# Kernel tuning notes

Hardware: AMD Instinct MI355X
Metric: run time of the kernel (lower is better)

Reference implementation:

```python
import jax, jax.numpy as jnp
import numpy as np

B, S, C = 16, 1024, 1024
E, H = 1024, 16
DH = E // H

def setup_inputs() -> dict:
    key = jax.random.key(0)
    k1, k2, k3, k4, k5 = jax.random.split(key, 5)
    x = jax.random.normal(k1, (B, S, C), dtype=jnp.float32)
    # learned params, sized per init_kwargs (torch Linear default init scale ~ 1/sqrt(fan_in))
    w_qkv = jax.random.normal(k2, (C, 3 * E), dtype=jnp.float32) / np.sqrt(C)
    b_qkv = jax.random.normal(k3, (3 * E,), dtype=jnp.float32) * 0.01
    w_o = jax.random.normal(k4, (E, E), dtype=jnp.float32) / np.sqrt(E)
    b_o = jax.random.normal(k5, (E,), dtype=jnp.float32) * 0.01
    return {"x": x, "w_qkv": w_qkv, "b_qkv": b_qkv, "w_o": w_o, "b_o": b_o}

def reference(x, w_qkv, b_qkv, w_o, b_o):
    b, s, _ = x.shape
    # fused QKV projection: [B,S,3E] -> [B,S,H,3*Dh]
    qkv = (jnp.einsum('bsc,ce->bse', x, w_qkv) + b_qkv).reshape(b, s, H, 3 * DH)
    q, k, v = jnp.split(qkv, 3, axis=-1)  # each [B,S,H,Dh]
    # NOTE: faithful to source — attention over the HEADS axis at each position,
    # scaled by embed_size**-0.5 (not head_dim).
    attn = jnp.einsum('bshd,bstd->bsht', q, k) * (E ** -0.5)  # [B,S,H,H]
    attn = jax.nn.softmax(attn, axis=-1)
    out = jnp.einsum('bsht,bstd->bshd', attn, v).reshape(b, s, E)
    return jnp.einsum('bse,ef->bsf', out, w_o) + b_o
```

## Files before the change

### kernel.cpp

```cpp
#include <hip/hip_runtime.h>
#include <hip/hip_bf16.h>
#include <stdint.h>

#define DEVINLINE __device__ __forceinline__

typedef __attribute__((ext_vector_type(4))) float f32x4;
typedef __attribute__((ext_vector_type(8))) short bf16x8;

DEVINLINE unsigned short f2bf(float f) {
    union { float f; uint32_t u; } v; v.f = f;
    uint32_t u = v.u;
    uint32_t rounding = 0x7FFFu + ((u >> 16) & 1u);
    u += rounding;
    return (unsigned short)(u >> 16);
}

DEVINLINE float bf2f(unsigned short h) {
    union { uint32_t u; float f; } v; v.u = ((uint32_t)h) << 16;
    return v.f;
}

__global__ void cvt_f32_bf16(const float* __restrict__ in,
                             unsigned short* __restrict__ out, int n) {
    int i = (blockIdx.x * blockDim.x + threadIdx.x) * 4;
    int stride = gridDim.x * blockDim.x * 4;
    for (; i < n; i += stride) {
        float4 v = *reinterpret_cast<const float4*>(in + i);
        ushort4 o;
        o.x = f2bf(v.x); o.y = f2bf(v.y); o.z = f2bf(v.z); o.w = f2bf(v.w);
        *reinterpret_cast<ushort4*>(out + i) = o;
    }
}

__global__ void transpose_cvt(const float* __restrict__ in,
                              unsigned short* __restrict__ out,
                              int R, int Ccols) {
    __shared__ float tile[32][33];
    int c0 = blockIdx.x * 32, r0 = blockIdx.y * 32;
    int tx = threadIdx.x, ty = threadIdx.y;
    #pragma unroll
    for (int j = 0; j < 32; j += 8)
        tile[ty + j][tx] = in[(size_t)(r0 + ty + j) * Ccols + c0 + tx];
    __syncthreads();
    #pragma unroll
    for (int j = 0; j < 32; j += 8)
        out[(size_t)(c0 + ty + j) * R + r0 + tx] = f2bf(tile[tx][ty + j]);
}


#define GLD(srcp, dstp) __builtin_amdgcn_global_load_lds( \
    (const __attribute__((address_space(1))) void*)(srcp), \
    (__attribute__((address_space(3))) void*)(dstp), 16, 0, 0)

#define STAGE(P, regionUS, srcBase, row0, kkE) do { \
    const unsigned short* _s = (srcBase) + (size_t)(row0) * K + (kkE); \
    unsigned short* _d = lds + (P) * 32768 + (regionUS) + wid * 512; \
    GLD(_s, _d); GLD(_s + (size_t)64 * K, _d + 4096); } while (0)

#define RD_A(dst, AS0, AS1, h) do { _Pragma("unroll") \
    for (int _i = 0; _i < 4; ++_i) { \
        dst[_i][0] = *(const bf16x8*)((AS0) + ((h) * 8192 + _i * 2048)); \
        dst[_i][1] = *(const bf16x8*)((AS1) + ((h) * 8192 + _i * 2048)); } } while (0)

#define RD_B(dst, BS0, BS1, nh) do { _Pragma("unroll") \
    for (int _j = 0; _j < 2; ++_j) { \
        dst[_j][0] = *(const bf16x8*)((BS0) + ((nh) * 4096 + _j * 2048)); \
        dst[_j][1] = *(const bf16x8*)((BS1) + ((nh) * 4096 + _j * 2048)); } } while (0)

#define MMA(aX, bY, mh, nh) do { \
    __builtin_amdgcn_s_setprio(1); \
    _Pragma("unroll") for (int _i = 0; _i < 4; ++_i) { \
    _Pragma("unroll") for (int _j = 0; _j < 2; ++_j) { \
        acc[(mh)*4+_i][(nh)*2+_j] = __builtin_amdgcn_mfma_f32_16x16x32_bf16( \
            aX[_i][0], bY[_j][0], acc[(mh)*4+_i][(nh)*2+_j], 0, 0, 0); \
        acc[(mh)*4+_i][(nh)*2+_j] = __builtin_amdgcn_mfma_f32_16x16x32_bf16( \
            aX[_i][1], bY[_j][1], acc[(mh)*4+_i][(nh)*2+_j], 0, 0, 0); } } \
    __builtin_amdgcn_s_setprio(0); } while (0)

#define VM4 asm volatile("s_waitcnt vmcnt(4)" ::: "memory")
#define BAR() asm volatile("s_barrier" ::: "memory")

#define KTILE(AS0c, AS1c, BS0c, BS1c, AS0n, AS1n, BS0n, BS1n, Pc, kk) do { \
    MMA(aA, bA, 0, 0); \
    RD_B(bB, BS0c, BS1c, 1); \
    BAR(); \
    MMA(aA, bB, 0, 1); \
    RD_A(aB, AS0c, AS1c, 1); \
    VM4; BAR(); \
    MMA(aB, bA, 1, 0); \
    RD_B(bA, BS0n, BS1n, 0); \
    STAGE(Pc, 16384, bSrc, 0,   kk); \
    STAGE(Pc, 24576, bSrc, 128, kk); \
    VM4; BAR(); \
    MMA(aB, bB, 1, 1); \
    RD_A(aA, AS0n, AS1n, 0); \
    STAGE(Pc, 0,     aSrc, 0,   kk); \
    STAGE(Pc, 8192,  aSrc, 128, kk); \
    BAR(); } while (0)

template <bool OUT_BF16>
__launch_bounds__(512, 2)
__global__ void gemm256(const unsigned short* __restrict__ A,
                        const unsigned short* __restrict__ Bt,
                        const float* __restrict__ bias,
                        void* __restrict__ Cout,
                        int M, int N, int K, int NTN) {
    __shared__ unsigned short lds[65536];
    const int NT = K >> 6;

    int t = threadIdx.x;
    int wid = t >> 6, lane = t & 63;
    int wr = wid >> 2, wc = wid & 3;
    int fr = lane & 15, fq = lane >> 4;

    int nwg = gridDim.x, bid = blockIdx.x;
    int cpx = nwg >> 3;
    int swz = (bid & 7) * cpx + (bid >> 3);
    int tm = swz / NTN, tn = swz % NTN;
    int bm = tm * 256, bn = tn * 256;

    int rowl = t >> 3, col8 = t & 7;
    int swzcol = (col8 ^ (rowl & 7)) << 3;
    const unsigned short* aSrc = A + (size_t)(bm + rowl) * K + swzcol;
    const unsigned short* bSrc = Bt + (size_t)(bn + rowl) * K + swzcol;

    int swzm = (fr & 7) << 3;
    int colS0 = (fq << 3) ^ swzm;
    int colS1 = (32 | (fq << 3)) ^ swzm;

    char* ldsb = (char*)lds;
    char* A00 = ldsb + ((wr * 128 + fr) << 7) + 2 * colS0;
    char* A10 = ldsb + ((wr * 128 + fr) << 7) + 2 * colS1;
    char* B00 = ldsb + ((256 + wc * 64 + fr) << 7) + 2 * colS0;
    char* B10 = ldsb + ((256 + wc * 64 + fr) << 7) + 2 * colS1;
    char* A01 = A00 + 65536; char* A11 = A10 + 65536;
    char* B01 = B00 + 65536; char* B11 = B10 + 65536;

    f32x4 acc[8][4] = {};
    bf16x8 aA[4][2], aB[4][2], bA[2][2], bB[2][2];

    STAGE(0, 0,     aSrc, 0,   0);
    STAGE(0, 8192,  aSrc, 128, 0);
    STAGE(0, 16384, bSrc, 0,   0);
    STAGE(0, 24576, bSrc, 128, 0);
    STAGE(1, 16384, bSrc, 0,   64);
    STAGE(1, 24576, bSrc, 128, 64);
    STAGE(1, 0,     aSrc, 0,   64);
    STAGE(1, 8192,  aSrc, 128, 64);
    asm volatile("s_waitcnt vmcnt(8)" ::: "memory");
    BAR();
    RD_A(aA, A00, A10, 0);
    RD_B(bA, B00, B10, 0);

    for (int tau = 0; tau < NT; tau += 2) {
        int kkA = ((tau + 2 < NT) ? (tau + 2) : (NT - 1)) << 6;
        KTILE(A00, A10, B00, B10, A01, A11, B01, B11, 0, kkA);
        int kkB = ((tau + 3 < NT) ? (tau + 3) : (NT - 1)) << 6;
        KTILE(A01, A11, B01, B11, A00, A10, B00, B10, 1, kkB);
    }
    asm volatile("s_waitcnt vmcnt(0)" ::: "memory");

    #pragma unroll
    for (int m = 0; m < 8; ++m) {
        #pragma unroll
        for (int n = 0; n < 4; ++n) {
            int col = bn + wc * 64 + n * 16 + fr;
            float bv = bias[col];
            #pragma unroll
            for (int r = 0; r < 4; ++r) {
                int row = bm + wr * 128 + m * 16 + fq * 4 + r;
                float v = acc[m][n][r] + bv;
                if (OUT_BF16)
                    ((unsigned short*)Cout)[(size_t)row * N + col] = f2bf(v);
                else
                    ((float*)Cout)[(size_t)row * N + col] = v;
            }
        }
    }
}

__global__ __launch_bounds__(64)
void attn_kernel(const unsigned short* __restrict__ qkv,
                 unsigned short* __restrict__ out) {
    __shared__ float sq[16][65], sk[16][65], sv[16][65];
    __shared__ float sp[16][17];
    int pos = blockIdx.x;
    int t = threadIdx.x;
    const unsigned short* rowp = qkv + (size_t)pos * 3072;

    #pragma unroll
    for (int j = 0; j < 6; ++j) {
        int f = (j * 64 + t) * 8;
        ushort4 v0 = *reinterpret_cast<const ushort4*>(rowp + f);
        ushort4 v1 = *reinterpret_cast<const ushort4*>(rowp + f + 4);
        float vals[8] = {bf2f(v0.x), bf2f(v0.y), bf2f(v0.z), bf2f(v0.w),
                         bf2f(v1.x), bf2f(v1.y), bf2f(v1.z), bf2f(v1.w)};
        int h = f / 192;
        int r = f % 192;
        float* dst = (r < 64) ? &sq[h][r] : (r < 128) ? &sk[h][r - 64] : &sv[h][r - 128];
        #pragma unroll
        for (int i = 0; i < 8; ++i) dst[i] = vals[i];
    }
    __syncthreads();

    int h = t >> 2;
    int tq = t & 3;
    float s[4];
    #pragma unroll
    for (int jj = 0; jj < 4; ++jj) {
        int tt = tq * 4 + jj;
        float acc = 0.f;
        for (int d = 0; d < 64; ++d) acc += sq[h][d] * sk[tt][d];
        s[jj] = acc * 0.03125f;
    }
    float m = fmaxf(fmaxf(s[0], s[1]), fmaxf(s[2], s[3]));
    m = fmaxf(m, __shfl_xor(m, 1));
    m = fmaxf(m, __shfl_xor(m, 2));
    float e[4], sum = 0.f;
    #pragma unroll
    for (int jj = 0; jj < 4; ++jj) { e[jj] = __expf(s[jj] - m); sum += e[jj]; }
    sum += __shfl_xor(sum, 1);
    sum += __shfl_xor(sum, 2);
    float inv = 1.0f / sum;
    #pragma unroll
    for (int jj = 0; jj < 4; ++jj) sp[h][tq * 4 + jj] = e[jj] * inv;
    __syncthreads();

    int dbase = tq * 16;
    float o[16] = {};
    for (int tt = 0; tt < 16; ++tt) {
        float p = sp[h][tt];
        #pragma unroll
        for (int dd = 0; dd < 16; ++dd) o[dd] += p * sv[tt][dbase + dd];
    }
    unsigned short ob[16];
    #pragma unroll
    for (int dd = 0; dd < 16; ++dd) ob[dd] = f2bf(o[dd]);
    ushort4* po = (ushort4*)(out + (size_t)pos * 1024 + h * 64 + dbase);
    #pragma unroll
    for (int i = 0; i < 4; ++i) {
        ushort4 w = { ob[i*4+0], ob[i*4+1], ob[i*4+2], ob[i*4+3] };
        po[i] = w;
    }
}

extern "C" void kernel_launch(void* const* d_in, const int* in_sizes, int n_in,
                              void* d_out, int out_size, void* d_ws, size_t ws_size,
                              hipStream_t stream) {
    const float* x     = (const float*)d_in[0];
    const float* w_qkv = (const float*)d_in[1];
    const float* b_qkv = (const float*)d_in[2];
    const float* w_o   = (const float*)d_in[3];
    const float* b_o   = (const float*)d_in[4];
    float* out = (float*)d_out;

    const int C = 1024, E = 1024;
    const int M = 16 * 1024;
    const int N1 = 3 * E;

    char* ws = (char*)d_ws;
    unsigned short* xb    = (unsigned short*)ws;
    unsigned short* wqkvT = xb    + (size_t)M * C;
    unsigned short* qkv   = wqkvT + (size_t)N1 * C;
    unsigned short* woT   = qkv   + (size_t)M * N1;
    unsigned short* aout  = woT   + (size_t)E * E;

    cvt_f32_bf16<<<2048, 256, 0, stream>>>(x, xb, M * C);
    dim3 tb(32, 8);
    transpose_cvt<<<dim3(N1 / 32, C / 32), tb, 0, stream>>>(w_qkv, wqkvT, C, N1);
    transpose_cvt<<<dim3(E / 32, E / 32), tb, 0, stream>>>(w_o, woT, E, E);

    gemm256<true><<<dim3((M / 256) * (N1 / 256)), 512, 0, stream>>>(
        xb, wqkvT, b_qkv, qkv, M, N1, C, N1 / 256);
    attn_kernel<<<M, 64, 0, stream>>>(qkv, aout);
    gemm256<false><<<dim3((M / 256) * (E / 256)), 512, 0, stream>>>(
        aout, woT, b_o, out, M, E, E, E / 256);
}
```

Measured before the change: 225.8 us.

## Compute per-position head attention scores with MFMA and vectorize PV loop

The QK^T scores over the 16 heads at each position are now computed with two bf16 MFMA 16x16x32 instructions, using fragments loaded straight from global memory instead of staging Q and K in shared memory as fp32. Only V is staged, with a padded row stride so the PV loop can use float4 shared reads. This removes one barrier, most of the shared-memory traffic, and the scalar 64-length dot products. Softmax reductions now shuffle across the MFMA output layout, and the whole kernel is still one small 64-thread block per position.

New measurement: 192.1 us. 14.9% less time.

```diff
diff --git a/kernel.cpp b/kernel.cpp
--- a/kernel.cpp
+++ b/kernel.cpp
@@ -182,66 +182,72 @@
 __global__ __launch_bounds__(64)
 void attn_kernel(const unsigned short* __restrict__ qkv,
                  unsigned short* __restrict__ out) {
-    __shared__ float sq[16][65], sk[16][65], sv[16][65];
+    __shared__ float sv[16][68];
     __shared__ float sp[16][17];
     int pos = blockIdx.x;
-    int t = threadIdx.x;
+    int l = threadIdx.x;
     const unsigned short* rowp = qkv + (size_t)pos * 3072;
 
     #pragma unroll
-    for (int j = 0; j < 6; ++j) {
-        int f = (j * 64 + t) * 8;
-        ushort4 v0 = *reinterpret_cast<const ushort4*>(rowp + f);
-        ushort4 v1 = *reinterpret_cast<const ushort4*>(rowp + f + 4);
-        float vals[8] = {bf2f(v0.x), bf2f(v0.y), bf2f(v0.z), bf2f(v0.w),
-                         bf2f(v1.x), bf2f(v1.y), bf2f(v1.z), bf2f(v1.w)};
-        int h = f / 192;
-        int r = f % 192;
-        float* dst = (r < 64) ? &sq[h][r] : (r < 128) ? &sk[h][r - 64] : &sv[h][r - 128];
-        #pragma unroll
-        for (int i = 0; i < 8; ++i) dst[i] = vals[i];
-    }
+    for (int j = 0; j < 4; ++j) {
+        int i8 = (j * 64 + l) * 8;
+        int h = i8 >> 6, d = i8 & 63;
+        ushort4 v0 = *reinterpret_cast<const ushort4*>(rowp + h * 192 + 128 + d);
+        ushort4 v1 = *reinterpret_cast<const ushort4*>(rowp + h * 192 + 128 + d + 4);
+        sv[h][d + 0] = bf2f(v0.x); sv[h][d + 1] = bf2f(v0.y);
+        sv[h][d + 2] = bf2f(v0.z); sv[h][d + 3] = bf2f(v0.w);
+        sv[h][d + 4] = bf2f(v1.x); sv[h][d + 5] = bf2f(v1.y);
+        sv[h][d + 6] = bf2f(v1.z); sv[h][d + 7] = bf2f(v1.w);
+    }
+
+    int fr = l & 15, fq = l >> 4;
+    const unsigned short* hb = rowp + fr * 192 + fq * 8;
+    bf16x8 kf0 = *reinterpret_cast<const bf16x8*>(hb + 64);
+    bf16x8 kf1 = *reinterpret_cast<const bf16x8*>(hb + 96);
+    bf16x8 qf0 = *reinterpret_cast<const bf16x8*>(hb);
+    bf16x8 qf1 = *reinterpret_cast<const bf16x8*>(hb + 32);
+    f32x4 st = {};
+    st = __builtin_amdgcn_mfma_f32_16x16x32_bf16(kf0, qf0, st, 0, 0, 0);
+    st = __builtin_amdgcn_mfma_f32_16x16x32_bf16(kf1, qf1, st, 0, 0, 0);
+
+    float s0 = st[0] * 0.03125f, s1 = st[1] * 0.03125f;
+    float s2 = st[2] * 0.03125f, s3 = st[3] * 0.03125f;
+    float m = fmaxf(fmaxf(s0, s1), fmaxf(s2, s3));
+    m = fmaxf(m, __shfl_xor(m, 16));
+    m = fmaxf(m, __shfl_xor(m, 32));
+    float e0 = __expf(s0 - m), e1 = __expf(s1 - m);
+    float e2 = __expf(s2 - m), e3 = __expf(s3 - m);
+    float sum = e0 + e1 + e2 + e3;
+    sum += __shfl_xor(sum, 16);
+    sum += __shfl_xor(sum, 32);
+    float inv = 1.0f / sum;
+    sp[fr][fq * 4 + 0] = e0 * inv;
+    sp[fr][fq * 4 + 1] = e1 * inv;
+    sp[fr][fq * 4 + 2] = e2 * inv;
+    sp[fr][fq * 4 + 3] = e3 * inv;
     __syncthreads();
 
-    int h = t >> 2;
-    int tq = t & 3;
-    float s[4];
-    #pragma unroll
-    for (int jj = 0; jj < 4; ++jj) {
-        int tt = tq * 4 + jj;
-        float acc = 0.f;
-        for (int d = 0; d < 64; ++d) acc += sq[h][d] * sk[tt][d];
-        s[jj] = acc * 0.03125f;
-    }
-    float m = fmaxf(fmaxf(s[0], s[1]), fmaxf(s[2], s[3]));
-    m = fmaxf(m, __shfl_xor(m, 1));
-    m = fmaxf(m, __shfl_xor(m, 2));
-    float e[4], sum = 0.f;
-    #pragma unroll
-    for (int jj = 0; jj < 4; ++jj) { e[jj] = __expf(s[jj] - m); sum += e[jj]; }
-    sum += __shfl_xor(sum, 1);
-    sum += __shfl_xor(sum, 2);
-    float inv = 1.0f / sum;
-    #pragma unroll
-    for (int jj = 0; jj < 4; ++jj) sp[h][tq * 4 + jj] = e[jj] * inv;
-    __syncthreads();
-
+    int h2 = l >> 2, tq = l & 3;
     int dbase = tq * 16;
-    float o[16] = {};
+    float4 o0 = {}, o1 = {}, o2 = {}, o3 = {};
+    #pragma unroll
     for (int tt = 0; tt < 16; ++tt) {
-        float p = sp[h][tt];
-        #pragma unroll
-        for (int dd = 0; dd < 16; ++dd) o[dd] += p * sv[tt][dbase + dd];
-    }
-    unsigned short ob[16];
-    #pragma unroll
-    for (int dd = 0; dd < 16; ++dd) ob[dd] = f2bf(o[dd]);
-    ushort4* po = (ushort4*)(out + (size_t)pos * 1024 + h * 64 + dbase);
-    #pragma unroll
-    for (int i = 0; i < 4; ++i) {
-        ushort4 w = { ob[i*4+0], ob[i*4+1], ob[i*4+2], ob[i*4+3] };
-        po[i] = w;
-    }
+        float p = sp[h2][tt];
+        float4 v0 = *reinterpret_cast<const float4*>(&sv[tt][dbase + 0]);
+        float4 v1 = *reinterpret_cast<const float4*>(&sv[tt][dbase + 4]);
+        float4 v2 = *reinterpret_cast<const float4*>(&sv[tt][dbase + 8]);
+        float4 v3 = *reinterpret_cast<const float4*>(&sv[tt][dbase + 12]);
+        o0.x += p * v0.x; o0.y += p * v0.y; o0.z += p * v0.z; o0.w += p * v0.w;
+        o1.x += p * v1.x; o1.y += p * v1.y; o1.z += p * v1.z; o1.w += p * v1.w;
+        o2.x += p * v2.x; o2.y += p * v2.y; o2.z += p * v2.z; o2.w += p * v2.w;
+        o3.x += p * v3.x; o3.y += p * v3.y; o3.z += p * v3.z; o3.w += p * v3.w;
+    }
+    ushort4* po = (ushort4*)(out + (size_t)pos * 1024 + h2 * 64 + dbase);
+    ushort4 w0 = { f2bf(o0.x), f2bf(o0.y), f2bf(o0.z), f2bf(o0.w) };
+    ushort4 w1 = { f2bf(o1.x), f2bf(o1.y), f2bf(o1.z), f2bf(o1.w) };
+    ushort4 w2 = { f2bf(o2.x), f2bf(o2.y), f2bf(o2.z), f2bf(o2.w) };
+    ushort4 w3 = { f2bf(o3.x), f2bf(o3.y), f2bf(o3.z), f2bf(o3.w) };
+    po[0] = w0; po[1] = w1; po[2] = w2; po[3] = w3;
 }
 
 extern "C" void kernel_launch(void* const* d_in, const int* in_sizes, int n_in,
```
